# Performance work log

Measured on AMD Instinct MI355X. Metric: run time of the kernel, lower is better.

## Reference

```python
import jax, jax.numpy as jnp
import numpy as np

B, N, DIM, HEADS = 4, 1024, 768, 12
HIDDEN, E, TOPK = 3072, 8, 2
EPS = 1e-5  # nn.LayerNorm default


def _layernorm(x, g, b):
    mu = jnp.mean(x, axis=-1, keepdims=True)
    var = jnp.var(x, axis=-1, keepdims=True)
    return (x - mu) * jax.lax.rsqrt(var + EPS) * g + b


def setup_inputs() -> dict:
    key = jax.random.key(0)
    ks = jax.random.split(key, 10)
    s = 0.02
    return {
        "x": jax.random.normal(ks[0], (B, N, DIM), dtype=jnp.float32),
        "ln1_g": jnp.ones((DIM,), jnp.float32),
        "ln1_b": jnp.zeros((DIM,), jnp.float32),
        "qkv_w": jax.random.normal(ks[1], (3 * DIM, DIM), jnp.float32) * s,  # qkv_bias=False
        "proj_w": jax.random.normal(ks[2], (DIM, DIM), jnp.float32) * s,
        "proj_b": jnp.zeros((DIM,), jnp.float32),
        "ln2_g": jnp.ones((DIM,), jnp.float32),
        "ln2_b": jnp.zeros((DIM,), jnp.float32),
        "gate_w": jax.random.normal(ks[3], (E, DIM), jnp.float32) * s,
        "gate_b": jnp.zeros((E,), jnp.float32),
        "w1": jax.random.normal(ks[4], (E, HIDDEN, DIM), jnp.float32) * s,
        "b1": jnp.zeros((E, HIDDEN), jnp.float32),
        "w2": jax.random.normal(ks[5], (E, DIM, HIDDEN), jnp.float32) * s,
        "b2": jnp.zeros((E, DIM), jnp.float32),
    }


def reference(x, ln1_g, ln1_b, qkv_w, proj_w, proj_b, ln2_g, ln2_b,
              gate_w, gate_b, w1, b1, w2, b2):
    b, n, d = x.shape
    hd = d // HEADS
    scale = hd ** -0.5

    # ---- attention branch ----
    h = _layernorm(x, ln1_g, ln1_b)
    qkv = h @ qkv_w.T                                   # [B,N,3D]
    qkv = qkv.reshape(b, n, 3, HEADS, hd).transpose(2, 0, 3, 1, 4)
    q, k, v = qkv[0], qkv[1], qkv[2]                    # [B,H,N,hd]
    attn = jax.nn.softmax(jnp.einsum('bhnd,bhmd->bhnm', q, k) * scale, axis=-1)
    a = jnp.einsum('bhnm,bhmd->bhnd', attn, v)
    a = a.transpose(0, 2, 1, 3).reshape(b, n, d)
    a = a @ proj_w.T + proj_b
    x = x + a

    # ---- MoE branch (NaiveGate, top_k=2) ----
    h2 = _layernorm(x, ln2_g, ln2_b)
    t = h2.reshape(-1, d)                               # [T,D]
    T = t.shape[0]
    logits = t @ gate_w.T + gate_b                      # [T,E]
    top_val, top_idx = jax.lax.top_k(logits, TOPK)
    score = jax.nn.softmax(top_val, axis=-1)            # softmax over top-k logits
    # per-token combine weight for each expert, [T,E]
    cw = jnp.zeros((T, E), t.dtype).at[jnp.arange(T)[:, None], top_idx].add(score)

    out = jnp.zeros_like(t)
    for e in range(E):  # small fixed expert count; exact (no capacity drop)
        he = jax.nn.gelu(t @ w1[e].T + b1[e], approximate=False)
        ye = he @ w2[e].T + b2[e]
        out = out + cw[:, e:e + 1] * ye

    return x + out.reshape(b, n, d)
```

## Files before the change

kernel.cpp:

```cpp
#include <hip/hip_runtime.h>
#include <math.h>

typedef short s16x8 __attribute__((ext_vector_type(8)));
typedef float f32x4 __attribute__((ext_vector_type(4)));
typedef unsigned short u16x4 __attribute__((ext_vector_type(4)));
typedef unsigned short u16x8 __attribute__((ext_vector_type(8)));

#define DIM_ 768
#define HID_ 3072
#define NTOK 4096
#define CAP 9216

__device__ __forceinline__ unsigned short f2bf(float f) {
  unsigned u = __float_as_uint(f);
  u += 0x7fffu + ((u >> 16) & 1u);
  return (unsigned short)(u >> 16);
}
__device__ __forceinline__ float bf2f(unsigned short u) {
  return __uint_as_float(((unsigned)u) << 16);
}

__device__ __forceinline__ void async_cp16(const void* g, void* l) {
  __builtin_amdgcn_global_load_lds(
      (const __attribute__((address_space(1))) void*)g,
      (__attribute__((address_space(3))) void*)l, 16, 0, 0);
}

template<bool BBF>
__device__ __forceinline__ void gemm_tile(
    const unsigned short* __restrict__ A, int lda,
    const void* __restrict__ Bv, int ldb,
    int kbeg, int kend, int row0, int col0,
    unsigned short* lA, unsigned short* lB,
    f32x4 acc[4][4])
{
  const int tid = threadIdx.x;
  const int lane = tid & 63;
  const int w = tid >> 6;
  const int wm = (w >> 1) << 6;
  const int wn = (w & 1) << 6;
  const int g = lane >> 4;
  const int lm = lane & 15;

  for (int k0 = kbeg; k0 < kend; k0 += 32) {
    __syncthreads();
#pragma unroll
    for (int it = 0; it < 2; ++it) {
      int c = (w * 2 + it) * 64 + lane;
      int ar = c >> 2, ks = ((c & 3) ^ ((ar >> 1) & 3)) << 3;
      async_cp16(A + (size_t)(row0 + ar) * lda + (k0 + ks),
                 lA + (w * 2 + it) * 512);
    }
    if constexpr (BBF) {
      const unsigned short* Bb = (const unsigned short*)Bv;
#pragma unroll
      for (int it = 0; it < 2; ++it) {
        int c = (w * 2 + it) * 64 + lane;
        int br = c >> 2, ks = ((c & 3) ^ ((br >> 1) & 3)) << 3;
        async_cp16(Bb + (size_t)(col0 + br) * ldb + (k0 + ks),
                   lB + (w * 2 + it) * 512);
      }
    } else {
      const float* Bf = (const float*)Bv;
#pragma unroll
      for (int it = 0; it < 4; ++it) {
        int f = it * 1024 + tid * 4;
        int br = f >> 5, ke = f & 31;
        const float4 vv = *(const float4*)(Bf + (size_t)(col0 + br) * ldb + (k0 + ke));
        u16x4 pk;
        pk[0] = f2bf(vv.x); pk[1] = f2bf(vv.y); pk[2] = f2bf(vv.z); pk[3] = f2bf(vv.w);
        int ksw = (((ke >> 3) ^ ((br >> 1) & 3)) << 3) + (ke & 7);
        *(u16x4*)(lB + br * 32 + ksw) = pk;
      }
    }
    __syncthreads();
    s16x8 a_frag[4], b_frag[4];
#pragma unroll
    for (int mt = 0; mt < 4; ++mt) {
      int ra = wm + mt * 16 + lm;
      a_frag[mt] = *(const s16x8*)(lA + ra * 32 + ((g ^ ((ra >> 1) & 3)) << 3));
    }
#pragma unroll
    for (int nt = 0; nt < 4; ++nt) {
      int cb = wn + nt * 16 + lm;
      b_frag[nt] = *(const s16x8*)(lB + cb * 32 + ((g ^ ((cb >> 1) & 3)) << 3));
    }
#pragma unroll
    for (int mt = 0; mt < 4; ++mt)
#pragma unroll
      for (int nt = 0; nt < 4; ++nt)
        acc[mt][nt] = __builtin_amdgcn_mfma_f32_16x16x32_bf16(
            a_frag[mt], b_frag[nt], acc[mt][nt], 0, 0, 0);
  }
}

#define GEMM_PROLOGUE                                   \
  __shared__ unsigned short lA[128 * 32];               \
  __shared__ unsigned short lB[128 * 32];               \
  f32x4 acc[4][4];                                      \
  _Pragma("unroll") for (int a_ = 0; a_ < 4; ++a_)      \
  _Pragma("unroll") for (int b_ = 0; b_ < 4; ++b_) {    \
    acc[a_][b_][0]=0.f; acc[a_][b_][1]=0.f;             \
    acc[a_][b_][2]=0.f; acc[a_][b_][3]=0.f; }           \
  const int lane = threadIdx.x & 63;                    \
  const int w = threadIdx.x >> 6;                       \
  const int wm = (w >> 1) << 6, wn = (w & 1) << 6;      \
  const int g = lane >> 4, lm = lane & 15;


__global__ void k_cvt(const float* __restrict__ s, unsigned short* __restrict__ d, int n) {
  int i = (blockIdx.x * 256 + threadIdx.x) * 8;
  if (i >= n) return;
  float4 a = *(const float4*)(s + i);
  float4 b = *(const float4*)(s + i + 4);
  u16x8 o;
  o[0]=f2bf(a.x); o[1]=f2bf(a.y); o[2]=f2bf(a.z); o[3]=f2bf(a.w);
  o[4]=f2bf(b.x); o[5]=f2bf(b.y); o[6]=f2bf(b.z); o[7]=f2bf(b.w);
  *(u16x8*)(d + i) = o;
}

__global__ __launch_bounds__(256, 2) void k_qkv(
    const unsigned short* __restrict__ hbf, const unsigned short* __restrict__ qkvw,
    unsigned short* __restrict__ qkvb)
{
  GEMM_PROLOGUE
  int f = blockIdx.x, xcd = f & 7, s = f >> 3;
  int cg = s / 24, rr = (s % 24) / 6, c = cg * 6 + s % 6;
  int row0 = (xcd * 4 + rr) * 128, col0 = c * 128;
  gemm_tile<true>(hbf, DIM_, qkvw, DIM_, 0, DIM_, row0, col0, lA, lB, acc);
#pragma unroll
  for (int mt = 0; mt < 4; ++mt)
#pragma unroll
    for (int nt = 0; nt < 4; ++nt)
#pragma unroll
      for (int i = 0; i < 4; ++i) {
        int m = row0 + wm + mt * 16 + g * 4 + i;
        int n = col0 + wn + nt * 16 + lm;
        int which = (n >= 1536) ? 2 : (n >= 768 ? 1 : 0);
        int d = n - which * 768;
        int head = d >> 6, hd = d & 63;
        int b = m >> 10, nn = m & 1023;
        int bh = b * 12 + head;
        size_t addr = (which < 2)
            ? ((size_t)which * 3145728u + (size_t)bh * 65536u + (size_t)nn * 64 + hd)
            : (6291456u + (size_t)bh * 65536u + (size_t)hd * 1024 + nn);
        qkvb[addr] = f2bf(acc[mt][nt][i]);
      }
}

__global__ __launch_bounds__(256, 2) void k_attn(
    const unsigned short* __restrict__ qkv, unsigned short* __restrict__ abuf)
{
  __shared__ unsigned short lK[64 * 64];
  __shared__ unsigned short lV[64 * 64];
  __shared__ unsigned short lP[4][16 * 72];
  const int tid = threadIdx.x, lane = tid & 63, w = tid >> 6;
  const int g = lane >> 4, lm = lane & 15;
  const int f = blockIdx.x, xcd = f & 7, s = f >> 3;
  const int bh = xcd * 6 + (s >> 4);
  const int qt = s & 15;
  const unsigned short* qsec = qkv + (size_t)bh * 65536u;
  const unsigned short* ksec = qkv + 3145728u + (size_t)bh * 65536u;
  const unsigned short* vsec = qkv + 6291456u + (size_t)bh * 65536u;

  s16x8 bq[2];
  {
    const unsigned short* qp = qsec + (size_t)(qt * 64 + w * 16 + lm) * 64 + g * 8;
    bq[0] = *(const s16x8*)(qp);
    bq[1] = *(const s16x8*)(qp + 32);
  }
  f32x4 oacc[4];
#pragma unroll
  for (int dt = 0; dt < 4; ++dt) { oacc[dt][0]=0.f; oacc[dt][1]=0.f; oacc[dt][2]=0.f; oacc[dt][3]=0.f; }
  float m_i = -3.0e38f, l_i = 0.f;

  for (int kt = 0; kt < 16; ++kt) {
#pragma unroll
    for (int it = 0; it < 2; ++it) {
      int c = (w * 2 + it) * 64 + lane;
      int r = c >> 3, sl = (c & 7) ^ (r & 7);
      async_cp16(ksec + (size_t)(kt * 64 + r) * 64 + sl * 8, lK + (w * 2 + it) * 512);
      async_cp16(vsec + (size_t)r * 1024 + kt * 64 + sl * 8, lV + (w * 2 + it) * 512);
    }
    __syncthreads();
    f32x4 st[4];
#pragma unroll
    for (int mt = 0; mt < 4; ++mt) {
      f32x4 z; z[0]=0.f; z[1]=0.f; z[2]=0.f; z[3]=0.f;
#pragma unroll
      for (int ks = 0; ks < 2; ++ks) {
        int ra = mt * 16 + lm;
        s16x8 a = *(const s16x8*)(lK + ra * 64 + (((ks * 4 + g) ^ (ra & 7)) << 3));
        z = __builtin_amdgcn_mfma_f32_16x16x32_bf16(a, bq[ks], z, 0, 0, 0);
      }
      st[mt] = z;
    }
    float mx = -3.0e38f;
#pragma unroll
    for (int mt = 0; mt < 4; ++mt) {
      st[mt] *= 0.125f;
#pragma unroll
      for (int i = 0; i < 4; ++i) mx = fmaxf(mx, st[mt][i]);
    }
    mx = fmaxf(mx, __shfl_xor(mx, 16, 64));
    mx = fmaxf(mx, __shfl_xor(mx, 32, 64));
    float mnew = fmaxf(m_i, mx);
    float alpha = expf(m_i - mnew);
    float psum = 0.f;
#pragma unroll
    for (int mt = 0; mt < 4; ++mt) {
      u16x4 pk;
#pragma unroll
      for (int i = 0; i < 4; ++i) {
        float p = expf(st[mt][i] - mnew);
        psum += p;
        pk[i] = f2bf(p);
      }
      *(u16x4*)(&lP[w][lm * 72 + mt * 16 + g * 4]) = pk;
    }
    psum += __shfl_xor(psum, 16, 64);
    psum += __shfl_xor(psum, 32, 64);
    l_i = l_i * alpha + psum;
    m_i = mnew;
    __syncthreads();
    float al[4];
#pragma unroll
    for (int i = 0; i < 4; ++i) al[i] = __shfl(alpha, (lane & 48) | (g * 4 + i), 64);
#pragma unroll
    for (int dt = 0; dt < 4; ++dt) {
#pragma unroll
      for (int i = 0; i < 4; ++i) oacc[dt][i] *= al[i];
    }
#pragma unroll
    for (int ks = 0; ks < 2; ++ks) {
      s16x8 ap = *(const s16x8*)(&lP[w][lm * 72 + ks * 32 + g * 8]);
#pragma unroll
      for (int dt = 0; dt < 4; ++dt) {
        int rv = dt * 16 + lm;
        s16x8 bv = *(const s16x8*)(lV + rv * 64 + (((ks * 4 + g) ^ (rv & 7)) << 3));
        oacc[dt] = __builtin_amdgcn_mfma_f32_16x16x32_bf16(ap, bv, oacc[dt], 0, 0, 0);
      }
    }
    __syncthreads();
  }
  float linv[4];
#pragma unroll
  for (int i = 0; i < 4; ++i)
    linv[i] = 1.f / __shfl(l_i, (lane & 48) | (g * 4 + i), 64);
  int b = bh / 12, head = bh % 12;
#pragma unroll
  for (int dt = 0; dt < 4; ++dt)
#pragma unroll
    for (int i = 0; i < 4; ++i) {
      int q = qt * 64 + w * 16 + g * 4 + i;
      int col = head * 64 + dt * 16 + lm;
      abuf[(size_t)(b * 1024 + q) * DIM_ + col] = f2bf(oacc[dt][i] * linv[i]);
    }
}

__global__ __launch_bounds__(256, 2) void k_proj(
    const unsigned short* __restrict__ abuf, const unsigned short* __restrict__ projw,
    const float* __restrict__ projb, const float* __restrict__ x,
    float* __restrict__ x1)
{
  GEMM_PROLOGUE
  int row0 = blockIdx.x * 128, col0 = blockIdx.y * 128;
  gemm_tile<true>(abuf, DIM_, projw, DIM_, 0, DIM_, row0, col0, lA, lB, acc);
#pragma unroll
  for (int mt = 0; mt < 4; ++mt)
#pragma unroll
    for (int nt = 0; nt < 4; ++nt)
#pragma unroll
      for (int i = 0; i < 4; ++i) {
        int m = row0 + wm + mt * 16 + g * 4 + i;
        int n = col0 + wn + nt * 16 + lm;
        size_t idx = (size_t)m * DIM_ + n;
        x1[idx] = acc[mt][nt][i] + projb[n] + x[idx];
      }
}

template<bool BBF>
__global__ __launch_bounds__(256, 2) void k_ffn1(
    const unsigned short* __restrict__ xg, const void* __restrict__ w1,
    const float* __restrict__ b1, const int* __restrict__ off,
    unsigned short* __restrict__ hidden)
{
  int f = blockIdx.x, xcd = f & 7, s = f >> 3;
  int cg = s / 72, rr = (s % 72) >> 3, c = cg * 8 + (s & 7);
  int row0 = (xcd * 9 + rr) * 128, col0 = c * 128;
  if (row0 >= off[8]) return;
  int e = 0;
  while (!(row0 >= off[e] && row0 < off[e + 1])) ++e;
  GEMM_PROLOGUE
  const char* Bp = (const char*)w1 + (size_t)e * HID_ * DIM_ * (BBF ? 2 : 4);
  gemm_tile<BBF>(xg, DIM_, Bp, DIM_, 0, DIM_, row0, col0, lA, lB, acc);
#pragma unroll
  for (int mt = 0; mt < 4; ++mt)
#pragma unroll
    for (int nt = 0; nt < 4; ++nt)
#pragma unroll
      for (int i = 0; i < 4; ++i) {
        int m = row0 + wm + mt * 16 + g * 4 + i;
        int n = col0 + wn + nt * 16 + lm;
        float v = acc[mt][nt][i] + b1[e * HID_ + n];
        float ge = 0.5f * v * (1.f + erff(v * 0.70710678118654752f));
        hidden[(size_t)m * HID_ + n] = f2bf(ge);
      }
}

template<bool BBF>
__global__ __launch_bounds__(256, 2) void k_ffn2(
    const unsigned short* __restrict__ hidden, const void* __restrict__ w2,
    const float* __restrict__ b2, const int* __restrict__ off,
    unsigned short* __restrict__ ye0, unsigned short* __restrict__ ye1)
{
  int f = blockIdx.x, xcd = f & 7, s = f >> 3;
  int cg = s / 54, rem = s % 54;
  int rr = rem / 6, kk = (rem % 6) / 3, c = cg * 3 + rem % 3;
  int row0 = (xcd * 9 + rr) * 128, col0 = c * 128;
  if (row0 >= off[8]) return;
  int e = 0;
  while (!(row0 >= off[e] && row0 < off[e + 1])) ++e;
  GEMM_PROLOGUE
  const char* Bp = (const char*)w2 + (size_t)e * DIM_ * HID_ * (BBF ? 2 : 4);
  gemm_tile<BBF>(hidden, HID_, Bp, HID_, kk * 1536, kk * 1536 + 1536, row0, col0, lA, lB, acc);
  unsigned short* yh = kk ? ye1 : ye0;
#pragma unroll
  for (int mt = 0; mt < 4; ++mt)
#pragma unroll
    for (int nt = 0; nt < 4; ++nt)
#pragma unroll
      for (int i = 0; i < 4; ++i) {
        int m = row0 + wm + mt * 16 + g * 4 + i;
        int n = col0 + wn + nt * 16 + lm;
        float v = acc[mt][nt][i] + (kk ? 0.f : b2[e * DIM_ + n]);
        yh[(size_t)m * DIM_ + n] = f2bf(v);
      }
}

__global__ __launch_bounds__(256) void k_ln1(
    const float* __restrict__ x, const float* __restrict__ gg,
    const float* __restrict__ bb, unsigned short* __restrict__ out)
{
  int t = blockIdx.x, tid = threadIdx.x;
  const float* xr = x + (size_t)t * DIM_;
  float v0 = xr[tid], v1 = xr[tid + 256], v2 = xr[tid + 512];
  float s = v0 + v1 + v2, q = v0 * v0 + v1 * v1 + v2 * v2;
  for (int o = 32; o; o >>= 1) { s += __shfl_xor(s, o, 64); q += __shfl_xor(q, o, 64); }
  __shared__ float red[8];
  int lane = tid & 63, w = tid >> 6;
  if (!lane) { red[w] = s; red[4 + w] = q; }
  __syncthreads();
  s = red[0] + red[1] + red[2] + red[3];
  q = red[4] + red[5] + red[6] + red[7];
  float mean = s * (1.f / 768.f);
  float rstd = rsqrtf(q * (1.f / 768.f) - mean * mean + 1e-5f);
  unsigned short* orow = out + (size_t)t * DIM_;
  orow[tid]       = f2bf((v0 - mean) * rstd * gg[tid]       + bb[tid]);
  orow[tid + 256] = f2bf((v1 - mean) * rstd * gg[tid + 256] + bb[tid + 256]);
  orow[tid + 512] = f2bf((v2 - mean) * rstd * gg[tid + 512] + bb[tid + 512]);
}

__global__ __launch_bounds__(256) void k_ln2gate(
    const float* __restrict__ x1, const float* __restrict__ gg,
    const float* __restrict__ bb, const float* __restrict__ gw,
    const float* __restrict__ gb, unsigned short* __restrict__ h2,
    int* __restrict__ topidx, float* __restrict__ tops)
{
  int t = blockIdx.x, tid = threadIdx.x;
  const float* xr = x1 + (size_t)t * DIM_;
  float v0 = xr[tid], v1 = xr[tid + 256], v2 = xr[tid + 512];
  float s = v0 + v1 + v2, q = v0 * v0 + v1 * v1 + v2 * v2;
  for (int o = 32; o; o >>= 1) { s += __shfl_xor(s, o, 64); q += __shfl_xor(q, o, 64); }
  __shared__ float red[8];
  __shared__ float part[32];
  int lane = tid & 63, w = tid >> 6;
  if (!lane) { red[w] = s; red[4 + w] = q; }
  __syncthreads();
  s = red[0] + red[1] + red[2] + red[3];
  q = red[4] + red[5] + red[6] + red[7];
  float mean = s * (1.f / 768.f);
  float rstd = rsqrtf(q * (1.f / 768.f) - mean * mean + 1e-5f);
  float y0 = (v0 - mean) * rstd * gg[tid]       + bb[tid];
  float y1 = (v1 - mean) * rstd * gg[tid + 256] + bb[tid + 256];
  float y2 = (v2 - mean) * rstd * gg[tid + 512] + bb[tid + 512];
  unsigned short* hrow = h2 + (size_t)t * DIM_;
  hrow[tid] = f2bf(y0); hrow[tid + 256] = f2bf(y1); hrow[tid + 512] = f2bf(y2);
#pragma unroll
  for (int e = 0; e < 8; ++e) {
    float p = y0 * gw[e * DIM_ + tid] + y1 * gw[e * DIM_ + tid + 256] + y2 * gw[e * DIM_ + tid + 512];
    for (int o = 32; o; o >>= 1) p += __shfl_xor(p, o, 64);
    if (!lane) part[e * 4 + w] = p;
  }
  __syncthreads();
  if (tid == 0) {
    float lg[8];
#pragma unroll
    for (int e = 0; e < 8; ++e)
      lg[e] = part[e * 4] + part[e * 4 + 1] + part[e * 4 + 2] + part[e * 4 + 3] + gb[e];
    int i0 = 0; float b0 = lg[0];
#pragma unroll
    for (int e = 1; e < 8; ++e) if (lg[e] > b0) { b0 = lg[e]; i0 = e; }
    int i1 = (i0 == 0) ? 1 : 0; float b1v = lg[i1];
#pragma unroll
    for (int e = 0; e < 8; ++e)
      if (e != i0 && lg[e] > b1v) { b1v = lg[e]; i1 = e; }
    float e1 = expf(b1v - b0);
    float s0 = 1.f / (1.f + e1);
    topidx[t * 2] = i0; topidx[t * 2 + 1] = i1;
    tops[t * 2] = s0;  tops[t * 2 + 1] = e1 / (1.f + e1);
  }
}

__global__ void k_count(const int* __restrict__ topidx, int* __restrict__ cnt) {
  int i = blockIdx.x * 256 + threadIdx.x;
  atomicAdd(&cnt[topidx[i]], 1);
}

__global__ void k_offsets(const int* __restrict__ cnt, int* __restrict__ off) {
  if (threadIdx.x == 0) {
    int a = 0;
    for (int e = 0; e < 8; ++e) { off[e] = a; a += (cnt[e] + 127) & ~127; }
    off[8] = a;
  }
}

__global__ void k_scatter(const int* __restrict__ topidx, int* __restrict__ fill,
                          const int* __restrict__ off, int* __restrict__ pos_of) {
  int i = blockIdx.x * 256 + threadIdx.x;
  int e = topidx[i];
  pos_of[i] = off[e] + atomicAdd(&fill[e], 1);
}

__global__ void k_gather(const unsigned short* __restrict__ h2,
                         const int* __restrict__ pos_of,
                         unsigned short* __restrict__ xg) {
  int pair = blockIdx.x, tid = threadIdx.x;
  int pos = pos_of[pair], t = pair >> 1;
  ((uint2*)xg)[(size_t)pos * 192 + tid] = ((const uint2*)h2)[(size_t)t * 192 + tid];
}

__global__ void k_combine(const float* __restrict__ x1,
                          const unsigned short* __restrict__ y0h,
                          const unsigned short* __restrict__ y1h,
                          const int* __restrict__ pos_of, const float* __restrict__ tops,
                          float* __restrict__ out) {
  int t = blockIdx.x, tid = threadIdx.x;
  int p0 = pos_of[t * 2], p1 = pos_of[t * 2 + 1];
  float s0 = tops[t * 2], s1 = tops[t * 2 + 1];
  const float* xr = x1 + (size_t)t * DIM_;
  const unsigned short* a0 = y0h + (size_t)p0 * DIM_;
  const unsigned short* a1 = y1h + (size_t)p0 * DIM_;
  const unsigned short* b0 = y0h + (size_t)p1 * DIM_;
  const unsigned short* b1 = y1h + (size_t)p1 * DIM_;
  float* orow = out + (size_t)t * DIM_;
#pragma unroll
  for (int j = 0; j < 3; ++j) {
    int col = tid + j * 256;
    float ya = bf2f(a0[col]) + bf2f(a1[col]);
    float yb = bf2f(b0[col]) + bf2f(b1[col]);
    orow[col] = xr[col] + s0 * ya + s1 * yb;
  }
}

extern "C" void kernel_launch(void* const* d_in, const int* in_sizes, int n_in,
                              void* d_out, int out_size, void* d_ws, size_t ws_size,
                              hipStream_t stream) {
  const float* x     = (const float*)d_in[0];
  const float* ln1g  = (const float*)d_in[1];
  const float* ln1b  = (const float*)d_in[2];
  const float* qkvw  = (const float*)d_in[3];
  const float* projw = (const float*)d_in[4];
  const float* projb = (const float*)d_in[5];
  const float* ln2g  = (const float*)d_in[6];
  const float* ln2b  = (const float*)d_in[7];
  const float* gw    = (const float*)d_in[8];
  const float* gb    = (const float*)d_in[9];
  const float* w1    = (const float*)d_in[10];
  const float* b1    = (const float*)d_in[11];
  const float* w2    = (const float*)d_in[12];
  const float* b2    = (const float*)d_in[13];
  float* out = (float*)d_out;

  char* base = (char*)d_ws;
  unsigned short* hbf    = (unsigned short*)(base + 0);
  unsigned short* qkvb   = (unsigned short*)(base + 6291456);
  unsigned short* abuf   = (unsigned short*)(base + 25165824);
  float*          x1     = (float*)(base + 31457280);
  unsigned short* hidden = (unsigned short*)(base + 44040192);
  unsigned short* ye0    = (unsigned short*)(base + 100663296);
  unsigned short* ye1    = (unsigned short*)(base + 114819072);

  const size_t FULL_NEED = 209289320;
  const bool full = ws_size >= FULL_NEED;
  unsigned short *wqkvbf, *wprojbf, *w1bf = nullptr, *w2bf = nullptr;
  char* small;
  if (full) {
    wqkvbf  = (unsigned short*)(base + 128974848);
    wprojbf = (unsigned short*)(base + 132513792);
    w1bf    = (unsigned short*)(base + 133693440);
    w2bf    = (unsigned short*)(base + 171442176);
    small   = base + 209190912;
  } else {
    wqkvbf  = (unsigned short*)(base + 44040192);
    wprojbf = (unsigned short*)(base + 44040192 + 3538944);
    small   = base + 128974848;
  }
  int*   topidx = (int*)small;
  float* tops   = (float*)(small + 32768);
  int*   pos_of = (int*)(small + 65536);
  int*   cnt    = (int*)(small + 98304);
  int*   fill   = cnt + 8;
  int*   off    = (int*)(small + 98304 + 64);
  unsigned short* xg = qkvb;
  unsigned short* h2 = hbf;

  k_cvt<<<864, 256, 0, stream>>>(qkvw, wqkvbf, 3 * DIM_ * DIM_);
  k_cvt<<<288, 256, 0, stream>>>(projw, wprojbf, DIM_ * DIM_);
  if (full) {
    k_cvt<<<9216, 256, 0, stream>>>(w1, w1bf, 8 * HID_ * DIM_);
    k_cvt<<<9216, 256, 0, stream>>>(w2, w2bf, 8 * HID_ * DIM_);
  }
  k_ln1<<<NTOK, 256, 0, stream>>>(x, ln1g, ln1b, hbf);
  k_qkv<<<576, 256, 0, stream>>>(hbf, wqkvbf, qkvb);
  k_attn<<<768, 256, 0, stream>>>(qkvb, abuf);
  k_proj<<<dim3(32, 6), 256, 0, stream>>>(abuf, wprojbf, projb, x, x1);
  k_ln2gate<<<NTOK, 256, 0, stream>>>(x1, ln2g, ln2b, gw, gb, h2, topidx, tops);
  hipMemsetAsync(cnt, 0, 64, stream);
  k_count<<<32, 256, 0, stream>>>(topidx, cnt);
  k_offsets<<<1, 64, 0, stream>>>(cnt, off);
  hipMemsetAsync(xg, 0, (size_t)CAP * DIM_ * 2, stream);
  k_scatter<<<32, 256, 0, stream>>>(topidx, fill, off, pos_of);
  k_gather<<<8192, 192, 0, stream>>>(h2, pos_of, xg);
  if (full) {
    k_ffn1<true><<<1728, 256, 0, stream>>>(xg, w1bf, b1, off, hidden);
    k_ffn2<true><<<864, 256, 0, stream>>>(hidden, w2bf, b2, off, ye0, ye1);
  } else {
    k_ffn1<false><<<1728, 256, 0, stream>>>(xg, w1, b1, off, hidden);
    k_ffn2<false><<<864, 256, 0, stream>>>(hidden, w2, b2, off, ye0, ye1);
  }
  k_combine<<<NTOK, 256, 0, stream>>>(x1, ye0, ye1, pos_of, tops, out);
}
```

Baseline: 548.5 us.

## Double-buffer LDS in GEMM and attention loops, fuse routing and weight-convert kernels

The bf16 GEMM loop and the attention K/V loop now use two LDS buffers, issuing async global-to-LDS loads for the next k-tile while MFMAs run on the current one, and each iteration drops one barrier. The count/offset/scatter routing kernels and the memset are merged into a single 1024-thread block that uses shared-memory atomics. The four weight-conversion launches become one kernel. This doubles LDS per block, which may reduce occupancy, and it relies on the single barrier per iteration to order the async copies correctly.

```diff
diff --git a/kernel.cpp b/kernel.cpp
--- a/kernel.cpp
+++ b/kernel.cpp
@@ -27,7 +27,7 @@
 }
 
 template<bool BBF>
-__device__ __forceinline__ void gemm_tile(
+__device__ __forceinline__ void gemm_loop(
     const unsigned short* __restrict__ A, int lda,
     const void* __restrict__ Bv, int ldb,
     int kbeg, int kend, int row0, int col0,
@@ -42,26 +42,56 @@
   const int g = lane >> 4;
   const int lm = lane & 15;
 
-  for (int k0 = kbeg; k0 < kend; k0 += 32) {
-    __syncthreads();
-#pragma unroll
-    for (int it = 0; it < 2; ++it) {
-      int c = (w * 2 + it) * 64 + lane;
-      int ar = c >> 2, ks = ((c & 3) ^ ((ar >> 1) & 3)) << 3;
-      async_cp16(A + (size_t)(row0 + ar) * lda + (k0 + ks),
-                 lA + (w * 2 + it) * 512);
-    }
-    if constexpr (BBF) {
-      const unsigned short* Bb = (const unsigned short*)Bv;
+  if constexpr (BBF) {
+    const unsigned short* Bb = (const unsigned short*)Bv;
+    auto stage = [&](int k0, int p) {
 #pragma unroll
       for (int it = 0; it < 2; ++it) {
         int c = (w * 2 + it) * 64 + lane;
-        int br = c >> 2, ks = ((c & 3) ^ ((br >> 1) & 3)) << 3;
-        async_cp16(Bb + (size_t)(col0 + br) * ldb + (k0 + ks),
-                   lB + (w * 2 + it) * 512);
-      }
-    } else {
-      const float* Bf = (const float*)Bv;
+        int r = c >> 2, ks = ((c & 3) ^ ((r >> 1) & 3)) << 3;
+        async_cp16(A + (size_t)(row0 + r) * lda + (k0 + ks),
+                   lA + p * 4096 + (w * 2 + it) * 512);
+        async_cp16(Bb + (size_t)(col0 + r) * ldb + (k0 + ks),
+                   lB + p * 4096 + (w * 2 + it) * 512);
+      }
+    };
+    stage(kbeg, 0);
+    int p = 0;
+    for (int k0 = kbeg; k0 < kend; k0 += 32) {
+      __syncthreads();
+      if (k0 + 32 < kend) stage(k0 + 32, p ^ 1);
+      const unsigned short* bA = lA + p * 4096;
+      const unsigned short* bB = lB + p * 4096;
+      s16x8 a_frag[4], b_frag[4];
+#pragma unroll
+      for (int mt = 0; mt < 4; ++mt) {
+        int ra = wm + mt * 16 + lm;
+        a_frag[mt] = *(const s16x8*)(bA + ra * 32 + ((g ^ ((ra >> 1) & 3)) << 3));
+      }
+#pragma unroll
+      for (int nt = 0; nt < 4; ++nt) {
+        int cb = wn + nt * 16 + lm;
+        b_frag[nt] = *(const s16x8*)(bB + cb * 32 + ((g ^ ((cb >> 1) & 3)) << 3));
+      }
+#pragma unroll
+      for (int mt = 0; mt < 4; ++mt)
+#pragma unroll
+        for (int nt = 0; nt < 4; ++nt)
+          acc[mt][nt] = __builtin_amdgcn_mfma_f32_16x16x32_bf16(
+              a_frag[mt], b_frag[nt], acc[mt][nt], 0, 0, 0);
+      p ^= 1;
+    }
+  } else {
+    const float* Bf = (const float*)Bv;
+    for (int k0 = kbeg; k0 < kend; k0 += 32) {
+      __syncthreads();
+#pragma unroll
+      for (int it = 0; it < 2; ++it) {
+        int c = (w * 2 + it) * 64 + lane;
+        int r = c >> 2, ks = ((c & 3) ^ ((r >> 1) & 3)) << 3;
+        async_cp16(A + (size_t)(row0 + r) * lda + (k0 + ks),
+                   lA + (w * 2 + it) * 512);
+      }
 #pragma unroll
       for (int it = 0; it < 4; ++it) {
         int f = it * 1024 + tid * 4;
@@ -72,31 +102,31 @@
         int ksw = (((ke >> 3) ^ ((br >> 1) & 3)) << 3) + (ke & 7);
         *(u16x4*)(lB + br * 32 + ksw) = pk;
       }
-    }
-    __syncthreads();
-    s16x8 a_frag[4], b_frag[4];
-#pragma unroll
-    for (int mt = 0; mt < 4; ++mt) {
-      int ra = wm + mt * 16 + lm;
-      a_frag[mt] = *(const s16x8*)(lA + ra * 32 + ((g ^ ((ra >> 1) & 3)) << 3));
-    }
-#pragma unroll
-    for (int nt = 0; nt < 4; ++nt) {
-      int cb = wn + nt * 16 + lm;
-      b_frag[nt] = *(const s16x8*)(lB + cb * 32 + ((g ^ ((cb >> 1) & 3)) << 3));
-    }
-#pragma unroll
-    for (int mt = 0; mt < 4; ++mt)
-#pragma unroll
-      for (int nt = 0; nt < 4; ++nt)
-        acc[mt][nt] = __builtin_amdgcn_mfma_f32_16x16x32_bf16(
-            a_frag[mt], b_frag[nt], acc[mt][nt], 0, 0, 0);
+      __syncthreads();
+      s16x8 a_frag[4], b_frag[4];
+#pragma unroll
+      for (int mt = 0; mt < 4; ++mt) {
+        int ra = wm + mt * 16 + lm;
+        a_frag[mt] = *(const s16x8*)(lA + ra * 32 + ((g ^ ((ra >> 1) & 3)) << 3));
+      }
+#pragma unroll
+      for (int nt = 0; nt < 4; ++nt) {
+        int cb = wn + nt * 16 + lm;
+        b_frag[nt] = *(const s16x8*)(lB + cb * 32 + ((g ^ ((cb >> 1) & 3)) << 3));
+      }
+#pragma unroll
+      for (int mt = 0; mt < 4; ++mt)
+#pragma unroll
+        for (int nt = 0; nt < 4; ++nt)
+          acc[mt][nt] = __builtin_amdgcn_mfma_f32_16x16x32_bf16(
+              a_frag[mt], b_frag[nt], acc[mt][nt], 0, 0, 0);
+    }
   }
 }
 
 #define GEMM_PROLOGUE                                   \
-  __shared__ unsigned short lA[128 * 32];               \
-  __shared__ unsigned short lB[128 * 32];               \
+  __shared__ unsigned short lA[8192];                   \
+  __shared__ unsigned short lB[8192];                   \
   f32x4 acc[4][4];                                      \
   _Pragma("unroll") for (int a_ = 0; a_ < 4; ++a_)      \
   _Pragma("unroll") for (int b_ = 0; b_ < 4; ++b_) {    \
@@ -119,6 +149,24 @@
   *(u16x8*)(d + i) = o;
 }
 
+__global__ void k_cvt4(const float* __restrict__ s0, const float* __restrict__ s1,
+                       const float* __restrict__ s2, const float* __restrict__ s3,
+                       unsigned short* __restrict__ d0, unsigned short* __restrict__ d1,
+                       unsigned short* __restrict__ d2, unsigned short* __restrict__ d3) {
+  long i = (long)(blockIdx.x * 256 + threadIdx.x) * 8;
+  const float* s; unsigned short* d;
+  if (i < 1769472)             { s = s0;            d = d0; }
+  else if (i < 2359296)        { s = s1 - 1769472;  d = d1 - 1769472; }
+  else if (i < 21233664)       { s = s2 - 2359296;  d = d2 - 2359296; }
+  else                         { s = s3 - 21233664; d = d3 - 21233664; }
+  float4 a = *(const float4*)(s + i);
+  float4 b = *(const float4*)(s + i + 4);
+  u16x8 o;
+  o[0]=f2bf(a.x); o[1]=f2bf(a.y); o[2]=f2bf(a.z); o[3]=f2bf(a.w);
+  o[4]=f2bf(b.x); o[5]=f2bf(b.y); o[6]=f2bf(b.z); o[7]=f2bf(b.w);
+  *(u16x8*)(d + i) = o;
+}
+
 __global__ __launch_bounds__(256, 2) void k_qkv(
     const unsigned short* __restrict__ hbf, const unsigned short* __restrict__ qkvw,
     unsigned short* __restrict__ qkvb)
@@ -127,7 +175,7 @@
   int f = blockIdx.x, xcd = f & 7, s = f >> 3;
   int cg = s / 24, rr = (s % 24) / 6, c = cg * 6 + s % 6;
   int row0 = (xcd * 4 + rr) * 128, col0 = c * 128;
-  gemm_tile<true>(hbf, DIM_, qkvw, DIM_, 0, DIM_, row0, col0, lA, lB, acc);
+  gemm_loop<true>(hbf, DIM_, qkvw, DIM_, 0, DIM_, row0, col0, lA, lB, acc);
 #pragma unroll
   for (int mt = 0; mt < 4; ++mt)
 #pragma unroll
@@ -151,8 +199,8 @@
 __global__ __launch_bounds__(256, 2) void k_attn(
     const unsigned short* __restrict__ qkv, unsigned short* __restrict__ abuf)
 {
-  __shared__ unsigned short lK[64 * 64];
-  __shared__ unsigned short lV[64 * 64];
+  __shared__ unsigned short lK[2][4096];
+  __shared__ unsigned short lV[2][4096];
   __shared__ unsigned short lP[4][16 * 72];
   const int tid = threadIdx.x, lane = tid & 63, w = tid >> 6;
   const int g = lane >> 4, lm = lane & 15;
@@ -174,15 +222,20 @@
   for (int dt = 0; dt < 4; ++dt) { oacc[dt][0]=0.f; oacc[dt][1]=0.f; oacc[dt][2]=0.f; oacc[dt][3]=0.f; }
   float m_i = -3.0e38f, l_i = 0.f;
 
-  for (int kt = 0; kt < 16; ++kt) {
+  auto stage = [&](int kt, int p) {
 #pragma unroll
     for (int it = 0; it < 2; ++it) {
       int c = (w * 2 + it) * 64 + lane;
       int r = c >> 3, sl = (c & 7) ^ (r & 7);
-      async_cp16(ksec + (size_t)(kt * 64 + r) * 64 + sl * 8, lK + (w * 2 + it) * 512);
-      async_cp16(vsec + (size_t)r * 1024 + kt * 64 + sl * 8, lV + (w * 2 + it) * 512);
-    }
+      async_cp16(ksec + (size_t)(kt * 64 + r) * 64 + sl * 8, lK[p] + (w * 2 + it) * 512);
+      async_cp16(vsec + (size_t)r * 1024 + kt * 64 + sl * 8, lV[p] + (w * 2 + it) * 512);
+    }
+  };
+  stage(0, 0);
+  int p = 0;
+  for (int kt = 0; kt < 16; ++kt) {
     __syncthreads();
+    if (kt < 15) stage(kt + 1, p ^ 1);
     f32x4 st[4];
 #pragma unroll
     for (int mt = 0; mt < 4; ++mt) {
@@ -190,7 +243,7 @@
 #pragma unroll
       for (int ks = 0; ks < 2; ++ks) {
         int ra = mt * 16 + lm;
-        s16x8 a = *(const s16x8*)(lK + ra * 64 + (((ks * 4 + g) ^ (ra & 7)) << 3));
+        s16x8 a = *(const s16x8*)(lK[p] + ra * 64 + (((ks * 4 + g) ^ (ra & 7)) << 3));
         z = __builtin_amdgcn_mfma_f32_16x16x32_bf16(a, bq[ks], z, 0, 0, 0);
       }
       st[mt] = z;
@@ -212,9 +265,9 @@
       u16x4 pk;
 #pragma unroll
       for (int i = 0; i < 4; ++i) {
-        float p = expf(st[mt][i] - mnew);
-        psum += p;
-        pk[i] = f2bf(p);
+        float p2 = expf(st[mt][i] - mnew);
+        psum += p2;
+        pk[i] = f2bf(p2);
       }
       *(u16x4*)(&lP[w][lm * 72 + mt * 16 + g * 4]) = pk;
     }
@@ -222,7 +275,6 @@
     psum += __shfl_xor(psum, 32, 64);
     l_i = l_i * alpha + psum;
     m_i = mnew;
-    __syncthreads();
     float al[4];
 #pragma unroll
     for (int i = 0; i < 4; ++i) al[i] = __shfl(alpha, (lane & 48) | (g * 4 + i), 64);
@@ -237,11 +289,11 @@
 #pragma unroll
       for (int dt = 0; dt < 4; ++dt) {
         int rv = dt * 16 + lm;
-        s16x8 bv = *(const s16x8*)(lV + rv * 64 + (((ks * 4 + g) ^ (rv & 7)) << 3));
+        s16x8 bv = *(const s16x8*)(lV[p] + rv * 64 + (((ks * 4 + g) ^ (rv & 7)) << 3));
         oacc[dt] = __builtin_amdgcn_mfma_f32_16x16x32_bf16(ap, bv, oacc[dt], 0, 0, 0);
       }
     }
-    __syncthreads();
+    p ^= 1;
   }
   float linv[4];
 #pragma unroll
@@ -265,7 +317,7 @@
 {
   GEMM_PROLOGUE
   int row0 = blockIdx.x * 128, col0 = blockIdx.y * 128;
-  gemm_tile<true>(abuf, DIM_, projw, DIM_, 0, DIM_, row0, col0, lA, lB, acc);
+  gemm_loop<true>(abuf, DIM_, projw, DIM_, 0, DIM_, row0, col0, lA, lB, acc);
 #pragma unroll
   for (int mt = 0; mt < 4; ++mt)
 #pragma unroll
@@ -293,7 +345,7 @@
   while (!(row0 >= off[e] && row0 < off[e + 1])) ++e;
   GEMM_PROLOGUE
   const char* Bp = (const char*)w1 + (size_t)e * HID_ * DIM_ * (BBF ? 2 : 4);
-  gemm_tile<BBF>(xg, DIM_, Bp, DIM_, 0, DIM_, row0, col0, lA, lB, acc);
+  gemm_loop<BBF>(xg, DIM_, Bp, DIM_, 0, DIM_, row0, col0, lA, lB, acc);
 #pragma unroll
   for (int mt = 0; mt < 4; ++mt)
 #pragma unroll
@@ -323,7 +375,7 @@
   while (!(row0 >= off[e] && row0 < off[e + 1])) ++e;
   GEMM_PROLOGUE
   const char* Bp = (const char*)w2 + (size_t)e * DIM_ * HID_ * (BBF ? 2 : 4);
-  gemm_tile<BBF>(hidden, HID_, Bp, HID_, kk * 1536, kk * 1536 + 1536, row0, col0, lA, lB, acc);
+  gemm_loop<BBF>(hidden, HID_, Bp, HID_, kk * 1536, kk * 1536 + 1536, row0, col0, lA, lB, acc);
   unsigned short* yh = kk ? ye1 : ye0;
 #pragma unroll
   for (int mt = 0; mt < 4; ++mt)
@@ -412,24 +464,29 @@
   }
 }
 
-__global__ void k_count(const int* __restrict__ topidx, int* __restrict__ cnt) {
-  int i = blockIdx.x * 256 + threadIdx.x;
-  atomicAdd(&cnt[topidx[i]], 1);
-}
-
-__global__ void k_offsets(const int* __restrict__ cnt, int* __restrict__ off) {
-  if (threadIdx.x == 0) {
+__global__ __launch_bounds__(1024) void k_route(
+    const int* __restrict__ topidx, int* __restrict__ pos_of, int* __restrict__ off)
+{
+  __shared__ int scnt[8], soff[9], sfill[8];
+  int tid = threadIdx.x;
+  if (tid < 8) { scnt[tid] = 0; sfill[tid] = 0; }
+  __syncthreads();
+#pragma unroll
+  for (int j = 0; j < 8; ++j)
+    atomicAdd(&scnt[topidx[tid + j * 1024]], 1);
+  __syncthreads();
+  if (tid == 0) {
     int a = 0;
-    for (int e = 0; e < 8; ++e) { off[e] = a; a += (cnt[e] + 127) & ~127; }
-    off[8] = a;
-  }
-}
-
-__global__ void k_scatter(const int* __restrict__ topidx, int* __restrict__ fill,
-                          const int* __restrict__ off, int* __restrict__ pos_of) {
-  int i = blockIdx.x * 256 + threadIdx.x;
-  int e = topidx[i];
-  pos_of[i] = off[e] + atomicAdd(&fill[e], 1);
+    for (int e = 0; e < 8; ++e) { soff[e] = a; off[e] = a; a += (scnt[e] + 127) & ~127; }
+    soff[8] = a; off[8] = a;
+  }
+  __syncthreads();
+#pragma unroll
+  for (int j = 0; j < 8; ++j) {
+    int i = tid + j * 1024;
+    int e = topidx[i];
+    pos_of[i] = soff[e] + atomicAdd(&sfill[e], 1);
+  }
 }
 
 __global__ void k_gather(const unsigned short* __restrict__ h2,
@@ -509,28 +566,23 @@
   int*   topidx = (int*)small;
   float* tops   = (float*)(small + 32768);
   int*   pos_of = (int*)(small + 65536);
-  int*   cnt    = (int*)(small + 98304);
-  int*   fill   = cnt + 8;
-  int*   off    = (int*)(small + 98304 + 64);
+  int*   off    = (int*)(small + 98304);
   unsigned short* xg = qkvb;
   unsigned short* h2 = hbf;
 
-  k_cvt<<<864, 256, 0, stream>>>(qkvw, wqkvbf, 3 * DIM_ * DIM_);
-  k_cvt<<<288, 256, 0, stream>>>(projw, wprojbf, DIM_ * DIM_);
   if (full) {
-    k_cvt<<<9216, 256, 0, stream>>>(w1, w1bf, 8 * HID_ * DIM_);
-    k_cvt<<<9216, 256, 0, stream>>>(w2, w2bf, 8 * HID_ * DIM_);
+    k_cvt4<<<19584, 256, 0, stream>>>(qkvw, projw, w1, w2, wqkvbf, wprojbf, w1bf, w2bf);
+  } else {
+    k_cvt<<<864, 256, 0, stream>>>(qkvw, wqkvbf, 3 * DIM_ * DIM_);
+    k_cvt<<<288, 256, 0, stream>>>(projw, wprojbf, DIM_ * DIM_);
   }
   k_ln1<<<NTOK, 256, 0, stream>>>(x, ln1g, ln1b, hbf);
   k_qkv<<<576, 256, 0, stream>>>(hbf, wqkvbf, qkvb);
   k_attn<<<768, 256, 0, stream>>>(qkvb, abuf);
   k_proj<<<dim3(32, 6), 256, 0, stream>>>(abuf, wprojbf, projb, x, x1);
   k_ln2gate<<<NTOK, 256, 0, stream>>>(x1, ln2g, ln2b, gw, gb, h2, topidx, tops);
-  hipMemsetAsync(cnt, 0, 64, stream);
-  k_count<<<32, 256, 0, stream>>>(topidx, cnt);
-  k_offsets<<<1, 64, 0, stream>>>(cnt, off);
   hipMemsetAsync(xg, 0, (size_t)CAP * DIM_ * 2, stream);
-  k_scatter<<<32, 256, 0, stream>>>(topidx, fill, off, pos_of);
+  k_route<<<1, 1024, 0, stream>>>(topidx, pos_of, off);
   k_gather<<<8192, 192, 0, stream>>>(h2, pos_of, xg);
   if (full) {
     k_ffn1<true><<<1728, 256, 0, stream>>>(xg, w1bf, b1, off, hidden);
```

After: 488.4 us. -11.0%, faster.
